# Performance work log

Hardware: AMD Instinct MI355X
Metric: run time of the kernel (lower is better)

## Reference

```python
import jax, jax.numpy as jnp
import numpy as np

N = 200000
NNZ = 6400000
E = 500000
IN_P, IN_F, IN_N = 62, 37, 37
HID, LAT, DEC_HID = 256, 128, 64


def _p(key, shape, scale=0.05):
    return scale * jax.random.normal(key, shape, dtype=jnp.float32)


def setup_inputs() -> dict:
    key = jax.random.key(0)
    ks = jax.random.split(key, 32)
    inp = {
        'x_process': jax.random.normal(ks[0], (N, IN_P), dtype=jnp.float32),
        'x_file': jax.random.normal(ks[1], (N, IN_F), dtype=jnp.float32),
        'x_network': jax.random.normal(ks[2], (N, IN_N), dtype=jnp.float32),
        'adj_rows': jax.random.randint(ks[3], (NNZ,), 0, N, dtype=jnp.int32),
        'adj_cols': jax.random.randint(ks[4], (NNZ,), 0, N, dtype=jnp.int32),
        'adj_vals': jax.random.uniform(ks[5], (NNZ,), dtype=jnp.float32) / 32.0,
        'edge_src': jax.random.randint(ks[6], (E,), 0, N, dtype=jnp.int32),
        'edge_dst': jax.random.randint(ks[7], (E,), 0, N, dtype=jnp.int32),
        # per-view encoder params (weights stored [in, out])
        'Wp1': _p(ks[8], (IN_P, HID)), 'bp1': jnp.zeros((HID,), jnp.float32),
        'Wp2': _p(ks[9], (HID, LAT)), 'bp2': jnp.zeros((LAT,), jnp.float32),
        'Wf1': _p(ks[10], (IN_F, HID)), 'bf1': jnp.zeros((HID,), jnp.float32),
        'Wf2': _p(ks[11], (HID, LAT)), 'bf2': jnp.zeros((LAT,), jnp.float32),
        'Wn1': _p(ks[12], (IN_N, HID)), 'bn1': jnp.zeros((HID,), jnp.float32),
        'Wn2': _p(ks[13], (HID, LAT)), 'bn2': jnp.zeros((LAT,), jnp.float32),
        # gates
        'Wgp': _p(ks[14], (LAT, 1)), 'bgp': jnp.zeros((1,), jnp.float32),
        'Wgf': _p(ks[15], (LAT, 1)), 'bgf': jnp.zeros((1,), jnp.float32),
        'Wgn': _p(ks[16], (LAT, 1)), 'bgn': jnp.zeros((1,), jnp.float32),
        # mlp edge decoder
        'Wd1': _p(ks[17], (4 * LAT, DEC_HID)), 'bd1': jnp.zeros((DEC_HID,), jnp.float32),
        'Wd2': _p(ks[18], (DEC_HID, 1)), 'bd2': jnp.zeros((1,), jnp.float32),
    }
    return inp


def _spmm(rows, cols, vals, x):
    # sparse (COO) adjacency @ dense x : gather cols, scale, scatter-add into rows
    return jax.ops.segment_sum(vals[:, None] * x[cols], rows, num_segments=N)


def _encode_view(x, rows, cols, vals, W1, b1, W2, b2):
    h = jax.nn.relu(_spmm(rows, cols, vals, x) @ W1 + b1)  # dropout=0 / eval mode
    return _spmm(rows, cols, vals, h) @ W2 + b2


def reference(x_process, x_file, x_network, adj_rows, adj_cols, adj_vals,
              edge_src, edge_dst,
              Wp1, bp1, Wp2, bp2, Wf1, bf1, Wf2, bf2, Wn1, bn1, Wn2, bn2,
              Wgp, bgp, Wgf, bgf, Wgn, bgn, Wd1, bd1, Wd2, bd2):
    zp = _encode_view(x_process, adj_rows, adj_cols, adj_vals, Wp1, bp1, Wp2, bp2)
    zf = _encode_view(x_file, adj_rows, adj_cols, adj_vals, Wf1, bf1, Wf2, bf2)
    zn = _encode_view(x_network, adj_rows, adj_cols, adj_vals, Wn1, bn1, Wn2, bn2)
    # multi-view softmax gating -> fused latent [N, LAT]
    scores = jnp.concatenate([zp @ Wgp + bgp, zf @ Wgf + bgf, zn @ Wgn + bgn], axis=1)
    alpha = jax.nn.softmax(scores, axis=1)
    z = alpha[:, 0:1] * zp + alpha[:, 1:2] * zf + alpha[:, 2:3] * zn
    # mlp edge decoder: gather src/dst, concat features, small MLP
    zs, zd = z[edge_src], z[edge_dst]
    feats = jnp.concatenate([zs, zd, zs * zd, jnp.abs(zs - zd)], axis=1)  # [E, 4*LAT]
    logits = jax.nn.relu(feats @ Wd1 + bd1) @ Wd2 + bd2
    return logits[:, 0]
```

## Files before the change

### kernel.cpp

```cpp
#include <hip/hip_runtime.h>
#include <math.h>

#define Nn 200000
#define NNZV 6400000
#define NE 500000
#define HID 256
#define LAT 128

typedef _Float16 h2 __attribute__((ext_vector_type(2)));
typedef _Float16 f16x8 __attribute__((ext_vector_type(8)));
typedef float f32x4 __attribute__((ext_vector_type(4)));
typedef short s16x8 __attribute__((ext_vector_type(8)));
struct alignas(8) H4 { _Float16 h[4]; };

__device__ __forceinline__ float fdot2(h2 a, h2 b, float c){
  return __builtin_amdgcn_fdot2(a, b, c, false);
}
__device__ __forceinline__ h2 bch2(unsigned u){ return __builtin_bit_cast(h2, u); }

__global__ __launch_bounds__(256) void k_zero(int* __restrict__ cnt){
  int i = blockIdx.x*256 + threadIdx.x;
  if(i < Nn) cnt[i] = 0;
}

__global__ __launch_bounds__(256) void k_count(const int* __restrict__ rows, int* __restrict__ cnt){
  int i = blockIdx.x*256 + threadIdx.x;
  if(i < NNZV) atomicAdd(&cnt[rows[i]], 1);
}

__global__ __launch_bounds__(512) void k_scan_block(const int* __restrict__ cnt, int* __restrict__ incl, int* __restrict__ bsum){
  __shared__ int s[512];
  int t = threadIdx.x;
  int i = blockIdx.x*512 + t;
  int v = (i < Nn) ? cnt[i] : 0;
  s[t] = v; __syncthreads();
  for(int off = 1; off < 512; off <<= 1){
    int x = (t >= off) ? s[t-off] : 0;
    __syncthreads();
    s[t] += x;
    __syncthreads();
  }
  if(i < Nn) incl[i] = s[t];
  if(t == 511) bsum[blockIdx.x] = s[t];
}

__global__ __launch_bounds__(512) void k_scan_bsum(int* __restrict__ bsum, int nb){
  __shared__ int s[512];
  int t = threadIdx.x;
  int v = (t < nb) ? bsum[t] : 0;
  s[t] = v; __syncthreads();
  for(int off = 1; off < 512; off <<= 1){
    int x = (t >= off) ? s[t-off] : 0;
    __syncthreads();
    s[t] += x;
    __syncthreads();
  }
  if(t < nb) bsum[t] = s[t] - v;
}

__global__ __launch_bounds__(256) void k_finish(const int* __restrict__ incl, const int* __restrict__ boff, int* __restrict__ row_ptr){
  int i = blockIdx.x*256 + threadIdx.x;
  if(i < Nn) row_ptr[i+1] = incl[i] + boff[i >> 9];
  if(i == 0) row_ptr[0] = 0;
}

__global__ __launch_bounds__(256) void k_initcur(const int* __restrict__ row_ptr, int* __restrict__ cur){
  int i = blockIdx.x*256 + threadIdx.x;
  if(i < Nn) cur[i] = row_ptr[i];
}

__global__ __launch_bounds__(256) void k_scatter(const int* __restrict__ rows, const int* __restrict__ cols,
    const float* __restrict__ vals, int* __restrict__ cur,
    int* __restrict__ cols_s, _Float16* __restrict__ vals_s){
  int i = blockIdx.x*256 + threadIdx.x;
  if(i >= NNZV) return;
  int r = rows[i];
  int j = atomicAdd(&cur[r], 1);
  cols_s[j] = cols[i];
  vals_s[j] = (_Float16)vals[i];
}

__global__ __launch_bounds__(256) void k_xpack(const float* __restrict__ xp, const float* __restrict__ xf,
    const float* __restrict__ xn, _Float16* __restrict__ xc){
  int idx = blockIdx.x*256 + threadIdx.x;
  int row = idx/36, c4 = idx - row*36;
  int cb = c4*4;
  H4 h;
  #pragma unroll
  for(int q = 0; q < 4; q++){
    int c = cb + q;
    float x;
    if(c < 62)       x = xp[row*62 + c];
    else if(c < 99)  x = xf[row*37 + (c-62)];
    else if(c == 99) x = 0.f;
    else if(c < 137) x = xn[row*37 + (c-100)];
    else             x = 0.f;
    h.h[q] = (_Float16)x;
  }
  *(H4*)&xc[row*144 + cb] = h;
}

__global__ __launch_bounds__(256) void k_wpack(
    const float* __restrict__ Wp1, const float* __restrict__ Wf1, const float* __restrict__ Wn1,
    const float* __restrict__ Wp2, const float* __restrict__ Wf2, const float* __restrict__ Wn2,
    h2* __restrict__ w1p, h2* __restrict__ w1f, h2* __restrict__ w1n,
    h2* __restrict__ w2p, h2* __restrict__ w2f, h2* __restrict__ w2n){
  int i = blockIdx.x*256 + threadIdx.x;
  const float* src; h2* dst; int K, C, idx;
  if(i < 7936)      { src=Wp1; dst=w1p; K=62;  C=256; idx=i; }
  else if(i < 12800){ src=Wf1; dst=w1f; K=37;  C=256; idx=i-7936; }
  else if(i < 17664){ src=Wn1; dst=w1n; K=37;  C=256; idx=i-12800; }
  else if(i < 34048){ src=Wp2; dst=w2p; K=256; C=128; idx=i-17664; }
  else if(i < 50432){ src=Wf2; dst=w2f; K=256; C=128; idx=i-34048; }
  else if(i < 66816){ src=Wn2; dst=w2n; K=256; C=128; idx=i-50432; }
  else return;
  int j = idx / C, c = idx - j*C;
  float a = src[(2*j)*C + c];
  float b = (2*j+1 < K) ? src[(2*j+1)*C + c] : 0.f;
  h2 r; r[0] = (_Float16)a; r[1] = (_Float16)b;
  dst[idx] = r;
}

__global__ void k_const(const float* b2p, const float* Wgp, const float* bgp,
                        const float* b2f, const float* Wgf, const float* bgf,
                        const float* b2n, const float* Wgn, const float* bgn,
                        float* c3){
  int l = threadIdx.x;
  float p = 0.f, f = 0.f, n = 0.f;
  for(int j = l; j < LAT; j += 64){
    p += b2p[j]*Wgp[j];
    f += b2f[j]*Wgf[j];
    n += b2n[j]*Wgn[j];
  }
  #pragma unroll
  for(int off = 32; off >= 1; off >>= 1){
    p += __shfl_xor(p, off);
    f += __shfl_xor(f, off);
    n += __shfl_xor(n, off);
  }
  if(l == 0){ c3[0] = p + bgp[0]; c3[1] = f + bgf[0]; c3[2] = n + bgn[0]; }
}

template<int NPAIR>
__device__ __forceinline__ void encode_view(
    int tid, int row0, int voff, int vidx,
    const _Float16 (*sT)[144], _Float16 (*hT)[HID],
    const h2* __restrict__ W1h, const float* __restrict__ b1,
    const h2* __restrict__ W2h, const float* __restrict__ Wg,
    _Float16* __restrict__ Yv, float* __restrict__ yg4f){
  {
    int c0 = (tid & 63)*4, rg = (tid >> 6)*8;
    float4 acc[8];
    #pragma unroll
    for(int i = 0; i < 8; i++) acc[i] = make_float4(0.f,0.f,0.f,0.f);
    for(int j = 0; j < NPAIR; j++){
      uint4 wv = *(const uint4*)&W1h[j*HID + c0];
      h2 w0 = bch2(wv.x), w1 = bch2(wv.y), w2 = bch2(wv.z), w3 = bch2(wv.w);
      #pragma unroll
      for(int i = 0; i < 8; i++){
        h2 s2 = *(const h2*)&sT[rg + i][voff + 2*j];
        acc[i].x = fdot2(s2, w0, acc[i].x);
        acc[i].y = fdot2(s2, w1, acc[i].y);
        acc[i].z = fdot2(s2, w2, acc[i].z);
        acc[i].w = fdot2(s2, w3, acc[i].w);
      }
    }
    float4 bb = *(const float4*)&b1[c0];
    #pragma unroll
    for(int i = 0; i < 8; i++){
      float h0 = fmaxf(acc[i].x + bb.x, 0.f);
      float h1 = fmaxf(acc[i].y + bb.y, 0.f);
      float h2v = fmaxf(acc[i].z + bb.z, 0.f);
      float h3 = fmaxf(acc[i].w + bb.w, 0.f);
      h2 t0; t0[0] = (_Float16)h0; t0[1] = (_Float16)h1;
      h2 t1; t1[0] = (_Float16)h2v; t1[1] = (_Float16)h3;
      *(h2*)&hT[rg + i][c0]     = t0;
      *(h2*)&hT[rg + i][c0 + 2] = t1;
    }
  }
  __syncthreads();
  {
    int c0 = (tid & 31)*4, rg = (tid >> 5)*4;
    float4 acc[4];
    #pragma unroll
    for(int i = 0; i < 4; i++) acc[i] = make_float4(0.f,0.f,0.f,0.f);
    for(int k2 = 0; k2 < HID/2; k2++){
      uint4 wv = *(const uint4*)&W2h[k2*LAT + c0];
      h2 w0 = bch2(wv.x), w1 = bch2(wv.y), w2 = bch2(wv.z), w3 = bch2(wv.w);
      #pragma unroll
      for(int i = 0; i < 4; i++){
        h2 hh = *(const h2*)&hT[rg + i][2*k2];
        acc[i].x = fdot2(hh, w0, acc[i].x);
        acc[i].y = fdot2(hh, w1, acc[i].y);
        acc[i].z = fdot2(hh, w2, acc[i].z);
        acc[i].w = fdot2(hh, w3, acc[i].w);
      }
    }
    float4 wg = *(const float4*)&Wg[c0];
    #pragma unroll
    for(int i = 0; i < 4; i++){
      int row = row0 + rg + i;
      h2 t0; t0[0] = (_Float16)acc[i].x; t0[1] = (_Float16)acc[i].y;
      h2 t1; t1[0] = (_Float16)acc[i].z; t1[1] = (_Float16)acc[i].w;
      *(h2*)&Yv[(size_t)row*LAT + c0]     = t0;
      *(h2*)&Yv[(size_t)row*LAT + c0 + 2] = t1;
      float p = acc[i].x*wg.x + acc[i].y*wg.y + acc[i].z*wg.z + acc[i].w*wg.w;
      #pragma unroll
      for(int off = 16; off >= 1; off >>= 1) p += __shfl_xor(p, off);
      if((tid & 31) == 0) yg4f[(size_t)row*4 + vidx] = p;
    }
  }
  __syncthreads();
}

__global__ __launch_bounds__(256, 5) void k_encfused(
    const int* __restrict__ row_ptr, const int* __restrict__ cols_s, const _Float16* __restrict__ vals_s,
    const _Float16* __restrict__ xc,
    const h2* __restrict__ w1p, const float* __restrict__ bp1, const h2* __restrict__ w2p, const float* __restrict__ Wgp,
    const h2* __restrict__ w1f, const float* __restrict__ bf1, const h2* __restrict__ w2f, const float* __restrict__ Wgf,
    const h2* __restrict__ w1n, const float* __restrict__ bn1, const h2* __restrict__ w2n, const float* __restrict__ Wgn,
    _Float16* __restrict__ Yp, _Float16* __restrict__ Yf, _Float16* __restrict__ Yn,
    float* __restrict__ yg4f){
  __shared__ _Float16 sT[32][144];
  __shared__ _Float16 hT[32][HID];
  int tid = threadIdx.x;
  int lane = tid & 63, wid = tid >> 6;
  int row0 = blockIdx.x * 32;
  bool has2 = (lane < 16);

  for(int rr8 = 0; rr8 < 8; rr8++){
    int r = row0 + wid*8 + rr8;
    int start = row_ptr[r], end = row_ptr[r+1];
    float a0 = 0.f, a1 = 0.f, a2 = 0.f;
    for(int j0 = start; j0 < end; j0 += 64){
      int m = end - j0; if(m > 64) m = 64;
      int mycol = 0; float myval = 0.f;
      if(lane < m){ mycol = cols_s[j0 + lane]; myval = (float)vals_s[j0 + lane]; }
      int mpad = (m + 3) & ~3;
      for(int k = 0; k < mpad; k += 4){
        #pragma unroll
        for(int q = 0; q < 4; q++){
          int c = __shfl(mycol, k + q);
          float v = __shfl(myval, k + q);
          const _Float16* xr = &xc[(size_t)c*144];
          float x0 = (float)xr[lane];
          float x1 = (float)xr[64 + lane];
          a0 = fmaf(v, x0, a0);
          a1 = fmaf(v, x1, a1);
          if(has2){
            float x2 = (float)xr[128 + lane];
            a2 = fmaf(v, x2, a2);
          }
        }
      }
    }
    int rr = wid*8 + rr8;
    sT[rr][lane]      = (_Float16)a0;
    sT[rr][64 + lane] = (_Float16)a1;
    if(has2) sT[rr][128 + lane] = (_Float16)a2;
  }
  __syncthreads();

  encode_view<31>(tid, row0, 0,   0, sT, hT, w1p, bp1, w2p, Wgp, Yp, yg4f);
  encode_view<19>(tid, row0, 62,  1, sT, hT, w1f, bf1, w2f, Wgf, Yf, yg4f);
  encode_view<19>(tid, row0, 100, 2, sT, hT, w1n, bn1, w2n, Wgn, Yn, yg4f);
}

__global__ __launch_bounds__(256) void k_spmm2f(
    const int* __restrict__ row_ptr, const int* __restrict__ cols_s, const _Float16* __restrict__ vals_s,
    const _Float16* __restrict__ Yp, const _Float16* __restrict__ Yf, const _Float16* __restrict__ Yn,
    const float4* __restrict__ yg4, const float* __restrict__ c3,
    const float* __restrict__ b2p, const float* __restrict__ b2f, const float* __restrict__ b2n,
    _Float16* __restrict__ z){
  int tid = threadIdx.x;
  int hl = tid & 31;
  int base = tid & 32;
  int r = blockIdx.x*8 + (tid >> 5);
  int start = row_ptr[r], end = row_ptr[r+1];
  int o = hl*4;
  float ap0=0,ap1=0,ap2=0,ap3=0, af0=0,af1=0,af2=0,af3=0, an0=0,an1=0,an2=0,an3=0;
  float scp=0.f, scf=0.f, scn=0.f;
  for(int j0 = start; j0 < end; j0 += 32){
    int m = end - j0; if(m > 32) m = 32;
    int mycol = 0; float myval = 0.f;
    if(hl < m){
      mycol = cols_s[j0 + hl];
      myval = (float)vals_s[j0 + hl];
      float4 g = yg4[mycol];
      scp = fmaf(myval, g.x, scp);
      scf = fmaf(myval, g.y, scf);
      scn = fmaf(myval, g.z, scn);
    }
    int mpad = (m + 1) & ~1;
    for(int k = 0; k < mpad; k += 2){
      #pragma unroll
      for(int q = 0; q < 2; q++){
        int c = __shfl(mycol, base + k + q);
        float v = __shfl(myval, base + k + q);
        size_t b = (size_t)c*LAT + o;
        uint2 rp = *(const uint2*)&Yp[b];
        uint2 rf = *(const uint2*)&Yf[b];
        uint2 rn = *(const uint2*)&Yn[b];
        h2 pl = bch2(rp.x), ph = bch2(rp.y);
        h2 fl = bch2(rf.x), fh = bch2(rf.y);
        h2 nl = bch2(rn.x), nh = bch2(rn.y);
        ap0 = fmaf(v, (float)pl[0], ap0); ap1 = fmaf(v, (float)pl[1], ap1);
        ap2 = fmaf(v, (float)ph[0], ap2); ap3 = fmaf(v, (float)ph[1], ap3);
        af0 = fmaf(v, (float)fl[0], af0); af1 = fmaf(v, (float)fl[1], af1);
        af2 = fmaf(v, (float)fh[0], af2); af3 = fmaf(v, (float)fh[1], af3);
        an0 = fmaf(v, (float)nl[0], an0); an1 = fmaf(v, (float)nl[1], an1);
        an2 = fmaf(v, (float)nh[0], an2); an3 = fmaf(v, (float)nh[1], an3);
      }
    }
  }
  #pragma unroll
  for(int off = 16; off >= 1; off >>= 1){
    scp += __shfl_xor(scp, off);
    scf += __shfl_xor(scf, off);
    scn += __shfl_xor(scn, off);
  }
  float sp = scp + c3[0], sf = scf + c3[1], sn = scn + c3[2];
  float mx = fmaxf(sp, fmaxf(sf, sn));
  float ep = expf(sp - mx), ef = expf(sf - mx), en = expf(sn - mx);
  float inv = 1.f / (ep + ef + en);
  float A0 = ep*inv, A1 = ef*inv, A2 = en*inv;
  float4 bp = *(const float4*)&b2p[o];
  float4 bf = *(const float4*)&b2f[o];
  float4 bn = *(const float4*)&b2n[o];
  float z0 = A0*(ap0 + bp.x) + A1*(af0 + bf.x) + A2*(an0 + bn.x);
  float z1 = A0*(ap1 + bp.y) + A1*(af1 + bf.y) + A2*(an1 + bn.y);
  float z2 = A0*(ap2 + bp.z) + A1*(af2 + bf.z) + A2*(an2 + bn.z);
  float z3 = A0*(ap3 + bp.w) + A1*(af3 + bf.w) + A2*(an3 + bn.w);
  H4 outv;
  outv.h[0] = (_Float16)z0; outv.h[1] = (_Float16)z1;
  outv.h[2] = (_Float16)z2; outv.h[3] = (_Float16)z3;
  *(H4*)&z[(size_t)r*LAT + o] = outv;
}

#define DEC_TILES (NE/16)
__global__ __launch_bounds__(256) void k_dec(
    const _Float16* __restrict__ z, const int* __restrict__ esrc, const int* __restrict__ edst,
    const float* __restrict__ Wd1, const float* __restrict__ bd1,
    const float* __restrict__ Wd2, const float* __restrict__ bd2, float* __restrict__ out){
  __shared__ float part[4][16][68];
  int tid = threadIdx.x;
  int w  = tid >> 6;
  int l  = tid & 63;
  int erow = l & 15;
  int kg   = l >> 4;

  f16x8 bfr[4][4];
  #pragma unroll
  for(int kt = 0; kt < 4; kt++){
    #pragma unroll
    for(int nt = 0; nt < 4; nt++){
      f16x8 bb;
      #pragma unroll
      for(int j = 0; j < 8; j++)
        bb[j] = (_Float16)Wd1[(w*128 + kt*32 + kg*8 + j)*64 + nt*16 + erow];
      bfr[kt][nt] = bb;
    }
  }

  int n0 = (tid & 15) * 4;
  int e2 = tid >> 4;
  float4 bb1 = *(const float4*)&bd1[n0];
  float4 w2v = *(const float4*)&Wd2[n0];
  float bias2 = bd2[0];

  for(int tile = blockIdx.x; tile < DEC_TILES; tile += gridDim.x){
    int e = tile*16 + erow;
    int si = esrc[e], di = edst[e];
    const f16x8* zs = (const f16x8*)&z[(size_t)si*LAT];
    const f16x8* zd = (const f16x8*)&z[(size_t)di*LAT];
    f16x8 afr[4];
    if(w == 0){
      #pragma unroll
      for(int kt = 0; kt < 4; kt++) afr[kt] = zs[kt*4 + kg];
    } else if(w == 1){
      #pragma unroll
      for(int kt = 0; kt < 4; kt++) afr[kt] = zd[kt*4 + kg];
    } else if(w == 2){
      #pragma unroll
      for(int kt = 0; kt < 4; kt++) afr[kt] = zs[kt*4 + kg] * zd[kt*4 + kg];
    } else {
      #pragma unroll
      for(int kt = 0; kt < 4; kt++){
        f16x8 d = zs[kt*4 + kg] - zd[kt*4 + kg];
        s16x8 m = __builtin_bit_cast(s16x8, d) & (short)0x7fff;
        afr[kt] = __builtin_bit_cast(f16x8, m);
      }
    }
    f32x4 zero = {0.f, 0.f, 0.f, 0.f};
    f32x4 acc[4] = {zero, zero, zero, zero};
    #pragma unroll
    for(int kt = 0; kt < 4; kt++){
      #pragma unroll
      for(int nt = 0; nt < 4; nt++)
        acc[nt] = __builtin_amdgcn_mfma_f32_16x16x32_f16(afr[kt], bfr[kt][nt], acc[nt], 0, 0, 0);
    }
    #pragma unroll
    for(int nt = 0; nt < 4; nt++){
      #pragma unroll
      for(int j = 0; j < 4; j++)
        part[w][kg*4 + j][nt*16 + erow] = acc[nt][j];
    }
    __syncthreads();
    float s0 = part[0][e2][n0+0] + part[1][e2][n0+0] + part[2][e2][n0+0] + part[3][e2][n0+0];
    float s1 = part[0][e2][n0+1] + part[1][e2][n0+1] + part[2][e2][n0+1] + part[3][e2][n0+1];
    float s2 = part[0][e2][n0+2] + part[1][e2][n0+2] + part[2][e2][n0+2] + part[3][e2][n0+2];
    float s3 = part[0][e2][n0+3] + part[1][e2][n0+3] + part[2][e2][n0+3] + part[3][e2][n0+3];
    float p = fmaxf(s0 + bb1.x, 0.f)*w2v.x + fmaxf(s1 + bb1.y, 0.f)*w2v.y
            + fmaxf(s2 + bb1.z, 0.f)*w2v.z + fmaxf(s3 + bb1.w, 0.f)*w2v.w;
    #pragma unroll
    for(int off = 1; off < 16; off <<= 1) p += __shfl_xor(p, off);
    if((tid & 15) == 0) out[tile*16 + e2] = p + bias2;
    __syncthreads();
  }
}

extern "C" void kernel_launch(void* const* d_in, const int* in_sizes, int n_in,
                              void* d_out, int out_size, void* d_ws, size_t ws_size,
                              hipStream_t stream) {
  const float* xp  = (const float*)d_in[0];
  const float* xf  = (const float*)d_in[1];
  const float* xn  = (const float*)d_in[2];
  const int* arows = (const int*)d_in[3];
  const int* acols = (const int*)d_in[4];
  const float* avals = (const float*)d_in[5];
  const int* esrc  = (const int*)d_in[6];
  const int* edst  = (const int*)d_in[7];
  const float* Wp1 = (const float*)d_in[8];  const float* bp1 = (const float*)d_in[9];
  const float* Wp2 = (const float*)d_in[10]; const float* bp2 = (const float*)d_in[11];
  const float* Wf1 = (const float*)d_in[12]; const float* bf1 = (const float*)d_in[13];
  const float* Wf2 = (const float*)d_in[14]; const float* bf2w = (const float*)d_in[15];
  const float* Wn1 = (const float*)d_in[16]; const float* bn1 = (const float*)d_in[17];
  const float* Wn2 = (const float*)d_in[18]; const float* bn2 = (const float*)d_in[19];
  const float* Wgp = (const float*)d_in[20]; const float* bgp = (const float*)d_in[21];
  const float* Wgf = (const float*)d_in[22]; const float* bgf = (const float*)d_in[23];
  const float* Wgn = (const float*)d_in[24]; const float* bgn = (const float*)d_in[25];
  const float* Wd1 = (const float*)d_in[26]; const float* bd1 = (const float*)d_in[27];
  const float* Wd2 = (const float*)d_in[28]; const float* bd2 = (const float*)d_in[29];
  float* out = (float*)d_out;
  (void)in_sizes; (void)n_in; (void)out_size; (void)ws_size;

  char* base = (char*)d_ws;
  size_t off = 0;
  auto alloc = [&](size_t nbytes) -> char* {
    off = (off + 255) & ~(size_t)255;
    char* p = base + off;
    off += nbytes;
    return p;
  };
  int*      row_ptr = (int*)     alloc((size_t)(Nn + 1) * 4);
  int*      cols_s  = (int*)     alloc((size_t)NNZV * 4);
  _Float16* vals_s  = (_Float16*)alloc((size_t)NNZV * 2);
  _Float16* xcat    = (_Float16*)alloc((size_t)Nn * 144 * 2);
  _Float16* Yp      = (_Float16*)alloc((size_t)Nn * LAT * 2);
  _Float16* Yf      = (_Float16*)alloc((size_t)Nn * LAT * 2);
  _Float16* Yn      = (_Float16*)alloc((size_t)Nn * LAT * 2);
  float*    yg4     = (float*)   alloc((size_t)Nn * 4 * 4);
  float*    c3      = (float*)   alloc(256);
  h2* w1p = (h2*)alloc(7936*4);  h2* w1f = (h2*)alloc(4864*4);  h2* w1n = (h2*)alloc(4864*4);
  h2* w2p = (h2*)alloc(16384*4); h2* w2f = (h2*)alloc(16384*4); h2* w2n = (h2*)alloc(16384*4);
  _Float16* z = xcat;
  int* cur  = (int*)((char*)xcat);
  int* incl = (int*)((char*)xcat + 1000000);
  int* bsum = (int*)((char*)xcat + 2000000);

  int NB = (Nn + 511) / 512;

  k_zero   <<<(Nn + 255)/256, 256, 0, stream>>>(cur);
  k_count  <<<(NNZV + 255)/256, 256, 0, stream>>>(arows, cur);
  k_scan_block<<<NB, 512, 0, stream>>>(cur, incl, bsum);
  k_scan_bsum<<<1, 512, 0, stream>>>(bsum, NB);
  k_finish <<<(Nn + 255)/256, 256, 0, stream>>>(incl, bsum, row_ptr);
  k_initcur<<<(Nn + 255)/256, 256, 0, stream>>>(row_ptr, cur);
  k_scatter<<<(NNZV + 255)/256, 256, 0, stream>>>(arows, acols, avals, cur, cols_s, vals_s);

  k_xpack<<<(Nn*36 + 255)/256, 256, 0, stream>>>(xp, xf, xn, xcat);
  k_wpack<<<(66816 + 255)/256, 256, 0, stream>>>(Wp1, Wf1, Wn1, Wp2, Wf2, Wn2,
                                                 w1p, w1f, w1n, w2p, w2f, w2n);
  k_const<<<1, 64, 0, stream>>>(bp2, Wgp, bgp, bf2w, Wgf, bgf, bn2, Wgn, bgn, c3);

  k_encfused<<<Nn/32, 256, 0, stream>>>(row_ptr, cols_s, vals_s, xcat,
      w1p, bp1, w2p, Wgp,  w1f, bf1, w2f, Wgf,  w1n, bn1, w2n, Wgn,
      Yp, Yf, Yn, yg4);

  k_spmm2f<<<Nn/8, 256, 0, stream>>>(row_ptr, cols_s, vals_s, Yp, Yf, Yn,
      (const float4*)yg4, c3, bp2, bf2w, bn2, z);

  k_dec<<<2048, 256, 0, stream>>>(z, esrc, edst, Wd1, bd1, Wd2, bd2, out);
}
```

Baseline: 2.618 ms.

## Split packed features into 256B-aligned head plus tail, use readlane in SpMM gathers

The packed fp16 input features are split into a 128-column array with 256-byte rows plus a 16-column tail, so each neighbour gather reads one aligned 256-byte line with h2 loads per lane. Both SpMM loops now broadcast the column and value with readlane into scalar registers instead of using shuffles. The second SpMM switches from two 32-lane half-waves per row to one full wave per row, with each lane handling two columns. The occupancy hint on the fused encoder is removed. Together these aim to cut gather transactions and shuffle overhead, at the cost of narrower per-lane loads and fewer rows in flight per wave.

```diff
diff --git a/kernel.cpp b/kernel.cpp
--- a/kernel.cpp
+++ b/kernel.cpp
@@ -17,6 +17,9 @@
   return __builtin_amdgcn_fdot2(a, b, c, false);
 }
 __device__ __forceinline__ h2 bch2(unsigned u){ return __builtin_bit_cast(h2, u); }
+__device__ __forceinline__ float rdlanef(float v, int k){
+  return __uint_as_float(__builtin_amdgcn_readlane(__float_as_uint(v), k));
+}
 
 __global__ __launch_bounds__(256) void k_zero(int* __restrict__ cnt){
   int i = blockIdx.x*256 + threadIdx.x;
@@ -81,23 +84,30 @@
 }
 
 __global__ __launch_bounds__(256) void k_xpack(const float* __restrict__ xp, const float* __restrict__ xf,
-    const float* __restrict__ xn, _Float16* __restrict__ xc){
+    const float* __restrict__ xn, _Float16* __restrict__ xc0, _Float16* __restrict__ xtl){
   int idx = blockIdx.x*256 + threadIdx.x;
-  int row = idx/36, c4 = idx - row*36;
-  int cb = c4*4;
-  H4 h;
+  int row = idx/18, c8 = idx - row*18;
+  if(row >= Nn) return;
+  H4 ha, hb;
   #pragma unroll
-  for(int q = 0; q < 4; q++){
-    int c = cb + q;
+  for(int q = 0; q < 8; q++){
+    int c = c8*8 + q;
     float x;
     if(c < 62)       x = xp[row*62 + c];
     else if(c < 99)  x = xf[row*37 + (c-62)];
     else if(c == 99) x = 0.f;
     else if(c < 137) x = xn[row*37 + (c-100)];
     else             x = 0.f;
-    h.h[q] = (_Float16)x;
-  }
-  *(H4*)&xc[row*144 + cb] = h;
+    if(q < 4) ha.h[q] = (_Float16)x; else hb.h[q-4] = (_Float16)x;
+  }
+  if(c8 < 16){
+    *(H4*)&xc0[(size_t)row*128 + c8*8]     = ha;
+    *(H4*)&xc0[(size_t)row*128 + c8*8 + 4] = hb;
+  } else {
+    int t = (c8-16)*8;
+    *(H4*)&xtl[(size_t)row*16 + t]     = ha;
+    *(H4*)&xtl[(size_t)row*16 + t + 4] = hb;
+  }
 }
 
 __global__ __launch_bounds__(256) void k_wpack(
@@ -213,9 +223,9 @@
   __syncthreads();
 }
 
-__global__ __launch_bounds__(256, 5) void k_encfused(
+__global__ __launch_bounds__(256) void k_encfused(
     const int* __restrict__ row_ptr, const int* __restrict__ cols_s, const _Float16* __restrict__ vals_s,
-    const _Float16* __restrict__ xc,
+    const _Float16* __restrict__ xc0, const _Float16* __restrict__ xtl,
     const h2* __restrict__ w1p, const float* __restrict__ bp1, const h2* __restrict__ w2p, const float* __restrict__ Wgp,
     const h2* __restrict__ w1f, const float* __restrict__ bf1, const h2* __restrict__ w2f, const float* __restrict__ Wgf,
     const h2* __restrict__ w1n, const float* __restrict__ bn1, const h2* __restrict__ w2n, const float* __restrict__ Wgn,
@@ -226,12 +236,12 @@
   int tid = threadIdx.x;
   int lane = tid & 63, wid = tid >> 6;
   int row0 = blockIdx.x * 32;
-  bool has2 = (lane < 16);
+  bool hast = (lane < 8);
 
   for(int rr8 = 0; rr8 < 8; rr8++){
     int r = row0 + wid*8 + rr8;
     int start = row_ptr[r], end = row_ptr[r+1];
-    float a0 = 0.f, a1 = 0.f, a2 = 0.f;
+    float a0 = 0.f, a1 = 0.f, a2 = 0.f, a3 = 0.f;
     for(int j0 = start; j0 < end; j0 += 64){
       int m = end - j0; if(m > 64) m = 64;
       int mycol = 0; float myval = 0.f;
@@ -240,24 +250,26 @@
       for(int k = 0; k < mpad; k += 4){
         #pragma unroll
         for(int q = 0; q < 4; q++){
-          int c = __shfl(mycol, k + q);
-          float v = __shfl(myval, k + q);
-          const _Float16* xr = &xc[(size_t)c*144];
-          float x0 = (float)xr[lane];
-          float x1 = (float)xr[64 + lane];
-          a0 = fmaf(v, x0, a0);
-          a1 = fmaf(v, x1, a1);
-          if(has2){
-            float x2 = (float)xr[128 + lane];
-            a2 = fmaf(v, x2, a2);
+          int c = __builtin_amdgcn_readlane(mycol, k + q);
+          float v = rdlanef(myval, k + q);
+          h2 xa = *(const h2*)((const char*)xc0 + (((unsigned)c) << 8) + lane*4);
+          a0 = fmaf((float)xa[0], v, a0);
+          a1 = fmaf((float)xa[1], v, a1);
+          if(hast){
+            h2 xb = *(const h2*)((const char*)xtl + ((unsigned)c)*32 + lane*4);
+            a2 = fmaf((float)xb[0], v, a2);
+            a3 = fmaf((float)xb[1], v, a3);
           }
         }
       }
     }
     int rr = wid*8 + rr8;
-    sT[rr][lane]      = (_Float16)a0;
-    sT[rr][64 + lane] = (_Float16)a1;
-    if(has2) sT[rr][128 + lane] = (_Float16)a2;
+    h2 s01; s01[0] = (_Float16)a0; s01[1] = (_Float16)a1;
+    *(h2*)&sT[rr][2*lane] = s01;
+    if(hast){
+      h2 s23; s23[0] = (_Float16)a2; s23[1] = (_Float16)a3;
+      *(h2*)&sT[rr][128 + 2*lane] = s23;
+    }
   }
   __syncthreads();
 
@@ -273,48 +285,41 @@
     const float* __restrict__ b2p, const float* __restrict__ b2f, const float* __restrict__ b2n,
     _Float16* __restrict__ z){
   int tid = threadIdx.x;
-  int hl = tid & 31;
-  int base = tid & 32;
-  int r = blockIdx.x*8 + (tid >> 5);
+  int lane = tid & 63;
+  int r = blockIdx.x*4 + (tid >> 6);
   int start = row_ptr[r], end = row_ptr[r+1];
-  int o = hl*4;
-  float ap0=0,ap1=0,ap2=0,ap3=0, af0=0,af1=0,af2=0,af3=0, an0=0,an1=0,an2=0,an3=0;
+  unsigned lo = lane*4;
+  float ap0=0.f, ap1=0.f, af0=0.f, af1=0.f, an0=0.f, an1=0.f;
   float scp=0.f, scf=0.f, scn=0.f;
-  for(int j0 = start; j0 < end; j0 += 32){
-    int m = end - j0; if(m > 32) m = 32;
+  for(int j0 = start; j0 < end; j0 += 64){
+    int m = end - j0; if(m > 64) m = 64;
     int mycol = 0; float myval = 0.f;
-    if(hl < m){
-      mycol = cols_s[j0 + hl];
-      myval = (float)vals_s[j0 + hl];
+    if(lane < m){
+      mycol = cols_s[j0 + lane];
+      myval = (float)vals_s[j0 + lane];
       float4 g = yg4[mycol];
       scp = fmaf(myval, g.x, scp);
       scf = fmaf(myval, g.y, scf);
       scn = fmaf(myval, g.z, scn);
     }
-    int mpad = (m + 1) & ~1;
-    for(int k = 0; k < mpad; k += 2){
-      #pragma unroll
-      for(int q = 0; q < 2; q++){
-        int c = __shfl(mycol, base + k + q);
-        float v = __shfl(myval, base + k + q);
-        size_t b = (size_t)c*LAT + o;
-        uint2 rp = *(const uint2*)&Yp[b];
-        uint2 rf = *(const uint2*)&Yf[b];
-        uint2 rn = *(const uint2*)&Yn[b];
-        h2 pl = bch2(rp.x), ph = bch2(rp.y);
-        h2 fl = bch2(rf.x), fh = bch2(rf.y);
-        h2 nl = bch2(rn.x), nh = bch2(rn.y);
-        ap0 = fmaf(v, (float)pl[0], ap0); ap1 = fmaf(v, (float)pl[1], ap1);
-        ap2 = fmaf(v, (float)ph[0], ap2); ap3 = fmaf(v, (float)ph[1], ap3);
-        af0 = fmaf(v, (float)fl[0], af0); af1 = fmaf(v, (float)fl[1], af1);
-        af2 = fmaf(v, (float)fh[0], af2); af3 = fmaf(v, (float)fh[1], af3);
-        an0 = fmaf(v, (float)nl[0], an0); an1 = fmaf(v, (float)nl[1], an1);
-        an2 = fmaf(v, (float)nh[0], an2); an3 = fmaf(v, (float)nh[1], an3);
+    int mpad = (m + 3) & ~3;
+    for(int k = 0; k < mpad; k += 4){
+      #pragma unroll
+      for(int q = 0; q < 4; q++){
+        int c = __builtin_amdgcn_readlane(mycol, k + q);
+        float v = rdlanef(myval, k + q);
+        unsigned vo = (((unsigned)c) << 8) + lo;
+        h2 yp = *(const h2*)((const char*)Yp + vo);
+        h2 yf = *(const h2*)((const char*)Yf + vo);
+        h2 yn = *(const h2*)((const char*)Yn + vo);
+        ap0 = fmaf((float)yp[0], v, ap0); ap1 = fmaf((float)yp[1], v, ap1);
+        af0 = fmaf((float)yf[0], v, af0); af1 = fmaf((float)yf[1], v, af1);
+        an0 = fmaf((float)yn[0], v, an0); an1 = fmaf((float)yn[1], v, an1);
       }
     }
   }
   #pragma unroll
-  for(int off = 16; off >= 1; off >>= 1){
+  for(int off = 32; off >= 1; off >>= 1){
     scp += __shfl_xor(scp, off);
     scf += __shfl_xor(scf, off);
     scn += __shfl_xor(scn, off);
@@ -324,17 +329,14 @@
   float ep = expf(sp - mx), ef = expf(sf - mx), en = expf(sn - mx);
   float inv = 1.f / (ep + ef + en);
   float A0 = ep*inv, A1 = ef*inv, A2 = en*inv;
-  float4 bp = *(const float4*)&b2p[o];
-  float4 bf = *(const float4*)&b2f[o];
-  float4 bn = *(const float4*)&b2n[o];
+  int o = lane*2;
+  float2 bp = *(const float2*)&b2p[o];
+  float2 bf = *(const float2*)&b2f[o];
+  float2 bn = *(const float2*)&b2n[o];
   float z0 = A0*(ap0 + bp.x) + A1*(af0 + bf.x) + A2*(an0 + bn.x);
   float z1 = A0*(ap1 + bp.y) + A1*(af1 + bf.y) + A2*(an1 + bn.y);
-  float z2 = A0*(ap2 + bp.z) + A1*(af2 + bf.z) + A2*(an2 + bn.z);
-  float z3 = A0*(ap3 + bp.w) + A1*(af3 + bf.w) + A2*(an3 + bn.w);
-  H4 outv;
-  outv.h[0] = (_Float16)z0; outv.h[1] = (_Float16)z1;
-  outv.h[2] = (_Float16)z2; outv.h[3] = (_Float16)z3;
-  *(H4*)&z[(size_t)r*LAT + o] = outv;
+  h2 uz; uz[0] = (_Float16)z0; uz[1] = (_Float16)z1;
+  *(h2*)&z[(size_t)r*LAT + o] = uz;
 }
 
 #define DEC_TILES (NE/16)
@@ -455,7 +457,8 @@
   int*      row_ptr = (int*)     alloc((size_t)(Nn + 1) * 4);
   int*      cols_s  = (int*)     alloc((size_t)NNZV * 4);
   _Float16* vals_s  = (_Float16*)alloc((size_t)NNZV * 2);
-  _Float16* xcat    = (_Float16*)alloc((size_t)Nn * 144 * 2);
+  _Float16* xcat0   = (_Float16*)alloc((size_t)Nn * 128 * 2);
+  _Float16* xtail   = (_Float16*)alloc((size_t)Nn * 16 * 2);
   _Float16* Yp      = (_Float16*)alloc((size_t)Nn * LAT * 2);
   _Float16* Yf      = (_Float16*)alloc((size_t)Nn * LAT * 2);
   _Float16* Yn      = (_Float16*)alloc((size_t)Nn * LAT * 2);
@@ -463,10 +466,10 @@
   float*    c3      = (float*)   alloc(256);
   h2* w1p = (h2*)alloc(7936*4);  h2* w1f = (h2*)alloc(4864*4);  h2* w1n = (h2*)alloc(4864*4);
   h2* w2p = (h2*)alloc(16384*4); h2* w2f = (h2*)alloc(16384*4); h2* w2n = (h2*)alloc(16384*4);
-  _Float16* z = xcat;
-  int* cur  = (int*)((char*)xcat);
-  int* incl = (int*)((char*)xcat + 1000000);
-  int* bsum = (int*)((char*)xcat + 2000000);
+  _Float16* z = xcat0;
+  int* cur  = (int*)((char*)xcat0);
+  int* incl = (int*)((char*)xcat0 + 1000000);
+  int* bsum = (int*)((char*)xcat0 + 2000000);
 
   int NB = (Nn + 511) / 512;
 
@@ -478,16 +481,16 @@
   k_initcur<<<(Nn + 255)/256, 256, 0, stream>>>(row_ptr, cur);
   k_scatter<<<(NNZV + 255)/256, 256, 0, stream>>>(arows, acols, avals, cur, cols_s, vals_s);
 
-  k_xpack<<<(Nn*36 + 255)/256, 256, 0, stream>>>(xp, xf, xn, xcat);
+  k_xpack<<<(Nn*18 + 255)/256, 256, 0, stream>>>(xp, xf, xn, xcat0, xtail);
   k_wpack<<<(66816 + 255)/256, 256, 0, stream>>>(Wp1, Wf1, Wn1, Wp2, Wf2, Wn2,
                                                  w1p, w1f, w1n, w2p, w2f, w2n);
   k_const<<<1, 64, 0, stream>>>(bp2, Wgp, bgp, bf2w, Wgf, bgf, bn2, Wgn, bgn, c3);
 
-  k_encfused<<<Nn/32, 256, 0, stream>>>(row_ptr, cols_s, vals_s, xcat,
+  k_encfused<<<Nn/32, 256, 0, stream>>>(row_ptr, cols_s, vals_s, xcat0, xtail,
       w1p, bp1, w2p, Wgp,  w1f, bf1, w2f, Wgf,  w1n, bn1, w2n, Wgn,
       Yp, Yf, Yn, yg4);
 
-  k_spmm2f<<<Nn/8, 256, 0, stream>>>(row_ptr, cols_s, vals_s, Yp, Yf, Yn,
+  k_spmm2f<<<Nn/4, 256, 0, stream>>>(row_ptr, cols_s, vals_s, Yp, Yf, Yn,
       (const float4*)yg4, c3, bp2, bf2w, bn2, z);
 
   k_dec<<<2048, 256, 0, stream>>>(z, esrc, edst, Wd1, bd1, Wd2, bd2, out);
```

New measurement: 2.830 ms. 8.1% more time.
